# Performance work log

Measured on AMD Instinct MI355X. Metric: run time of the kernel, lower is better.

The kernel has to match this reference:

```python
import jax, jax.numpy as jnp
import numpy as np

N_NODES = 50000
N_EDGES = 800000
D = 128


def setup_inputs() -> dict:
    key = jax.random.key(0)
    ks = jax.random.split(key, 6)
    x = jax.random.normal(ks[0], (N_NODES, D), dtype=jnp.float32)
    edge_index = jax.random.randint(ks[1], (2, N_EDGES), 0, N_NODES, dtype=jnp.int32)
    scale = 1.0 / np.sqrt(D)
    W0 = jax.random.normal(ks[2], (D, D), dtype=jnp.float32) * scale
    W1 = jax.random.normal(ks[3], (D, D), dtype=jnp.float32) * scale
    W2 = jax.random.normal(ks[4], (D, D), dtype=jnp.float32) * scale
    b0 = jnp.zeros((D,), jnp.float32)
    b1 = jnp.zeros((D,), jnp.float32)
    b2 = jnp.zeros((D,), jnp.float32)
    return {"x": x, "edge_index": edge_index, "W0": W0, "b0": b0,
            "W1": W1, "b1": b1, "W2": W2, "b2": b2}


def _gcn_norm(edge_index, n_nodes, dtype):
    # symmetric normalization D^-1/2 A D^-1/2, no self loops (add_self_loops=False)
    src, dst = edge_index[1], edge_index[0]  # adj_t: aggregate src -> dst
    deg = jax.ops.segment_sum(jnp.ones(src.shape, dtype), src, num_segments=n_nodes)
    dis = jnp.where(deg > 0, jax.lax.rsqrt(jnp.maximum(deg, 1.0)), 0.0)
    return src, dst, dis[src] * dis[dst]  # per-edge norm [E]


def _gcn_layer(x, W, b, src, dst, norm, n_nodes):
    h = x @ W                                   # [N, d_out]
    msg = h[src] * norm[:, None]                # gather + scale, [E, d_out]
    agg = jax.ops.segment_sum(msg, dst, num_segments=n_nodes)
    return agg + b


def reference(x, edge_index, W0, b0, W1, b1, W2, b2):
    n = x.shape[0]
    src, dst, norm = _gcn_norm(edge_index, n, x.dtype)
    h = jax.nn.relu(_gcn_layer(x, W0, b0, src, dst, norm, n))
    h = jax.nn.relu(_gcn_layer(h, W1, b1, src, dst, norm, n))
    return _gcn_layer(h, W2, b2, src, dst, norm, n)
```

## Files before the change

kernel.cpp:

```cpp
#include <hip/hip_runtime.h>
#include <hip/hip_bf16.h>

#define DFEAT 128
#define RSPLIT 16
#define SSPLIT 64

typedef __attribute__((ext_vector_type(8))) short short8;
typedef __attribute__((ext_vector_type(4))) float f32x4;

__device__ __forceinline__ ushort f2bf(float f) {
    uint u = __float_as_uint(f);
    u += 0x7FFF + ((u >> 16) & 1);
    return (ushort)(u >> 16);
}
__device__ __forceinline__ float bf_lo(uint v) { return __uint_as_float(v << 16); }
__device__ __forceinline__ float bf_hi(uint v) { return __uint_as_float(v & 0xFFFF0000u); }


__global__ __launch_bounds__(512) void histrank_kernel(const int* __restrict__ EI,
                                                       int* __restrict__ cnt_part,
                                                       int* __restrict__ deg_part,
                                                       int* __restrict__ erank,
                                                       int nedges, int nnodes,
                                                       int range, int slice) {
    extern __shared__ int lds[];
    int* hd = lds;
    int* hs = lds + range;
    const int r = blockIdx.x & (RSPLIT - 1);
    const int s = blockIdx.x / RSPLIT;
    const int base = r * range;
    for (int i = threadIdx.x; i < 2 * range; i += 512) lds[i] = 0;
    __syncthreads();

    const int e0 = s * slice;
    const int e1 = min(nedges, e0 + slice);
    for (int e = e0 + threadIdx.x; e < e1; e += 512) {
        int dst = EI[e];
        int src = EI[nedges + e];
        unsigned ud = (unsigned)(dst - base);
        unsigned us = (unsigned)(src - base);
        if (ud < (unsigned)range) erank[e] = atomicAdd(&hd[ud], 1);
        if (us < (unsigned)range) atomicAdd(&hs[us], 1);
    }
    __syncthreads();

    for (int i = threadIdx.x; i < range; i += 512) {
        int node = base + i;
        if (node < nnodes) {
            cnt_part[s * nnodes + node] = hd[i];
            deg_part[s * nnodes + node] = hs[i];
        }
    }
}

__global__ __launch_bounds__(1024) void scan1_kernel(int* __restrict__ cnt_part,
                                                     const int* __restrict__ deg_part,
                                                     int* __restrict__ offs,
                                                     int* __restrict__ bsums,
                                                     float* __restrict__ dis, int n) {
    __shared__ int sm[1024];
    int t = threadIdx.x;
    int g = blockIdx.x * 1024 + t;
    int c = 0;
    if (g < n) {
        int d = 0;
        #pragma unroll
        for (int s = 0; s < SSPLIT; ++s) {
            int v = cnt_part[s * n + g];
            cnt_part[s * n + g] = c;
            c += v;
            d += deg_part[s * n + g];
        }
        dis[g] = (d > 0) ? rsqrtf((float)d) : 0.0f;
    }
    sm[t] = c;
    __syncthreads();
    for (int off = 1; off < 1024; off <<= 1) {
        int add = (t >= off) ? sm[t - off] : 0;
        __syncthreads();
        sm[t] += add;
        __syncthreads();
    }
    if (g < n) offs[g + 1] = sm[t];
    if (t == 1023) bsums[blockIdx.x] = sm[1023];
}

__global__ __launch_bounds__(1024) void scan3_kernel(int* __restrict__ offs,
                                                     const int* __restrict__ bsums,
                                                     int n, int nb) {
    __shared__ int pre[64];
    int t = threadIdx.x;
    if (t < 64) {
        int v = (t < nb) ? bsums[t] : 0;
        for (int off = 1; off < 64; off <<= 1) {
            int u = __shfl_up(v, off);
            if (t >= off) v += u;
        }
        int ex = __shfl_up(v, 1);
        if (t == 0) ex = 0;
        pre[t] = ex;
    }
    __syncthreads();
    int add = pre[blockIdx.x];
    int g = blockIdx.x * 1024 + t;
    if (g < n) offs[g + 1] += add;
    if (blockIdx.x == 0 && t == 0) offs[0] = 0;
}

__global__ void fill_kernel(const int* __restrict__ EI, const int* __restrict__ offs,
                            const int* __restrict__ erank, const int* __restrict__ sprefix,
                            const float* __restrict__ dis, int2* __restrict__ edges,
                            int nedges, int nnodes, int slice) {
    int e = blockIdx.x * blockDim.x + threadIdx.x;
    if (e >= nedges) return;
    int dst = EI[e];
    int src = EI[nedges + e];
    int s = e / slice;
    int idx = offs[dst] + sprefix[s * nnodes + dst] + erank[e];
    float nm = dis[src] * dis[dst];
    edges[idx] = make_int2(src, __float_as_int(nm));
}

__global__ void prepw_kernel(const float* __restrict__ W0, const float* __restrict__ W1,
                             const float* __restrict__ W2, ushort* __restrict__ Wtb) {
    int i = blockIdx.x * 256 + threadIdx.x;
    int m = i >> 14, r = i & 16383;
    int n = r >> 7, k = r & 127;
    const float* W = (m == 0) ? W0 : (m == 1) ? W1 : W2;
    Wtb[i] = f2bf(W[k * DFEAT + n]);
}


template <int IN_F32>
__global__ __launch_bounds__(256) void gemm_mfma(const void* __restrict__ Xin,
                                                 const ushort* __restrict__ Wtb,
                                                 ushort* __restrict__ Hb, int nrows) {
    __shared__ ushort wlds[128 * 136];
    const int t = threadIdx.x;

    #pragma unroll
    for (int q = 0; q < 8; ++q) {
        int c = t + q * 256;
        int row = c >> 4, cr = c & 15;
        short8 v = *(const short8*)(Wtb + c * 8);
        *(short8*)(&wlds[row * 136 + cr * 8]) = v;
    }
    __syncthreads();

    const int lane = t & 63;
    const int r16 = lane & 15, g = lane >> 4;
    const int row = blockIdx.x * 64 + (t >> 6) * 16 + r16;
    const int srow = (row < nrows) ? row : (nrows - 1);

    short8 a[4];
    if (IN_F32) {
        const float* X = (const float*)Xin;
        #pragma unroll
        for (int kc = 0; kc < 4; ++kc) {
            const float* p = X + (size_t)srow * DFEAT + kc * 32 + g * 8;
            float4 f0 = *(const float4*)p;
            float4 f1 = *(const float4*)(p + 4);
            short8 s;
            s[0] = (short)f2bf(f0.x); s[1] = (short)f2bf(f0.y);
            s[2] = (short)f2bf(f0.z); s[3] = (short)f2bf(f0.w);
            s[4] = (short)f2bf(f1.x); s[5] = (short)f2bf(f1.y);
            s[6] = (short)f2bf(f1.z); s[7] = (short)f2bf(f1.w);
            a[kc] = s;
        }
    } else {
        const ushort* X = (const ushort*)Xin;
        #pragma unroll
        for (int kc = 0; kc < 4; ++kc)
            a[kc] = *(const short8*)(X + (size_t)srow * DFEAT + kc * 32 + g * 8);
    }

    f32x4 acc[8];
    #pragma unroll
    for (int nt = 0; nt < 8; ++nt) acc[nt] = (f32x4){0.f, 0.f, 0.f, 0.f};

    #pragma unroll
    for (int kc = 0; kc < 4; ++kc) {
        #pragma unroll
        for (int nt = 0; nt < 8; ++nt) {
            short8 b = *(const short8*)(&wlds[(nt * 16 + r16) * 136 + kc * 32 + g * 8]);
            acc[nt] = __builtin_amdgcn_mfma_f32_16x16x32_bf16(a[kc], b, acc[nt], 0, 0, 0);
        }
    }

    const int orow_base = blockIdx.x * 64 + (t >> 6) * 16 + g * 4;
    #pragma unroll
    for (int nt = 0; nt < 8; ++nt) {
        #pragma unroll
        for (int r = 0; r < 4; ++r) {
            int orow = orow_base + r;
            if (orow < nrows)
                Hb[(size_t)orow * DFEAT + nt * 16 + r16] = f2bf(acc[nt][r]);
        }
    }
}


template <int RELU, int OUT_F32>
__global__ __launch_bounds__(256) void agg_kernel(const ushort* __restrict__ H,
                                                  const int* __restrict__ offs,
                                                  const int2* __restrict__ edges,
                                                  const float* __restrict__ bias,
                                                  void* __restrict__ OUT, int nnodes) {
    int node = blockIdx.x * 4 + (threadIdx.x >> 6);
    if (node >= nnodes) return;
    int lane = threadIdx.x & 63;
    int half = lane >> 5;
    int l32 = lane & 31;
    int s = offs[node];
    int e = offs[node + 1];

    float a0 = 0.f, a1 = 0.f, a2 = 0.f, a3 = 0.f;
    float c0 = 0.f, c1 = 0.f, c2 = 0.f, c3 = 0.f;
    const ushort* __restrict__ Hp = H + l32 * 4;

    int i = s + half;
    for (; i + 2 < e; i += 4) {
        int2 er0 = edges[i];
        int2 er1 = edges[i + 2];
        uint2 v0 = *(const uint2*)(Hp + (size_t)er0.x * DFEAT);
        uint2 v1 = *(const uint2*)(Hp + (size_t)er1.x * DFEAT);
        float n0 = __int_as_float(er0.y);
        float n1 = __int_as_float(er1.y);
        a0 += n0 * bf_lo(v0.x); a1 += n0 * bf_hi(v0.x);
        a2 += n0 * bf_lo(v0.y); a3 += n0 * bf_hi(v0.y);
        c0 += n1 * bf_lo(v1.x); c1 += n1 * bf_hi(v1.x);
        c2 += n1 * bf_lo(v1.y); c3 += n1 * bf_hi(v1.y);
    }
    if (i < e) {
        int2 er0 = edges[i];
        uint2 v0 = *(const uint2*)(Hp + (size_t)er0.x * DFEAT);
        float n0 = __int_as_float(er0.y);
        a0 += n0 * bf_lo(v0.x); a1 += n0 * bf_hi(v0.x);
        a2 += n0 * bf_lo(v0.y); a3 += n0 * bf_hi(v0.y);
    }
    a0 += c0; a1 += c1; a2 += c2; a3 += c3;

    a0 += __shfl_xor(a0, 32);
    a1 += __shfl_xor(a1, 32);
    a2 += __shfl_xor(a2, 32);
    a3 += __shfl_xor(a3, 32);

    float4 b4 = *(const float4*)&bias[l32 * 4];
    a0 += b4.x; a1 += b4.y; a2 += b4.z; a3 += b4.w;
    if (RELU) {
        a0 = fmaxf(a0, 0.f); a1 = fmaxf(a1, 0.f);
        a2 = fmaxf(a2, 0.f); a3 = fmaxf(a3, 0.f);
    }
    if (half == 0) {
        if (OUT_F32) {
            *(float4*)((float*)OUT + (size_t)node * DFEAT + l32 * 4) =
                make_float4(a0, a1, a2, a3);
        } else {
            uint2 p;
            p.x = (uint)f2bf(a0) | ((uint)f2bf(a1) << 16);
            p.y = (uint)f2bf(a2) | ((uint)f2bf(a3) << 16);
            *(uint2*)((ushort*)OUT + (size_t)node * DFEAT + l32 * 4) = p;
        }
    }
}


extern "C" void kernel_launch(void* const* d_in, const int* in_sizes, int n_in,
                              void* d_out, int out_size, void* d_ws, size_t ws_size,
                              hipStream_t stream) {
    const float* x  = (const float*)d_in[0];
    const int*   EI = (const int*)d_in[1];
    const float* W0 = (const float*)d_in[2];
    const float* b0 = (const float*)d_in[3];
    const float* W1 = (const float*)d_in[4];
    const float* b1 = (const float*)d_in[5];
    const float* W2 = (const float*)d_in[6];
    const float* b2 = (const float*)d_in[7];
    float* out = (float*)d_out;

    const int N = in_sizes[0] / DFEAT;
    const int E = in_sizes[1] / 2;
    const int range = (N + RSPLIT - 1) / RSPLIT;
    const int slice = (E + SSPLIT - 1) / SSPLIT;

    char* w = (char*)d_ws;
    auto alloc = [&](size_t bytes) {
        void* p = (void*)w;
        w += (bytes + 255) & ~(size_t)255;
        return p;
    };
    int*    offs  = (int*)alloc((size_t)(N + 1) * 4);
    int*    bsums = (int*)alloc(64 * 4);
    float*  dis   = (float*)alloc((size_t)N * 4);
    int*    erank = (int*)alloc((size_t)E * 4);
    int2*   edges = (int2*)alloc((size_t)E * 8);
    ushort* Wtb   = (ushort*)alloc((size_t)3 * DFEAT * DFEAT * 2);
    ushort* hbuf  = (ushort*)alloc((size_t)N * DFEAT * 2);
    ushort* abuf  = (ushort*)alloc((size_t)N * DFEAT * 2);

    int* cnt_part = (int*)hbuf;
    int* deg_part = (int*)abuf;

    const int nb = (N + 1023) / 1024;

    prepw_kernel<<<(3 * DFEAT * DFEAT) / 256, 256, 0, stream>>>(W0, W1, W2, Wtb);
    histrank_kernel<<<RSPLIT * SSPLIT, 512, 2 * range * 4, stream>>>(
        EI, cnt_part, deg_part, erank, E, N, range, slice);
    scan1_kernel<<<nb, 1024, 0, stream>>>(cnt_part, deg_part, offs, bsums, dis, N);
    scan3_kernel<<<nb, 1024, 0, stream>>>(offs, bsums, N, nb);
    fill_kernel<<<(E + 255) / 256, 256, 0, stream>>>(EI, offs, erank, cnt_part, dis,
                                                     edges, E, N, slice);

    const int gemmGrid = (N + 63) / 64;
    const int aggGrid  = (N + 3) / 4;

    gemm_mfma<1><<<gemmGrid, 256, 0, stream>>>(x, Wtb, hbuf, N);
    agg_kernel<1, 0><<<aggGrid, 256, 0, stream>>>(hbuf, offs, edges, b0, abuf, N);
    gemm_mfma<0><<<gemmGrid, 256, 0, stream>>>(abuf, Wtb + DFEAT * DFEAT, hbuf, N);
    agg_kernel<1, 0><<<aggGrid, 256, 0, stream>>>(hbuf, offs, edges, b1, abuf, N);
    gemm_mfma<0><<<gemmGrid, 256, 0, stream>>>(abuf, Wtb + 2 * DFEAT * DFEAT, hbuf, N);
    agg_kernel<0, 1><<<aggGrid, 256, 0, stream>>>(hbuf, offs, edges, b2, out, N);
}
```

Baseline: 221.4 us.

## Factor GCN norm into per-node scaling and widen aggregation gathers

```diff
diff --git a/kernel.cpp b/kernel.cpp
--- a/kernel.cpp
+++ b/kernel.cpp
@@ -2,7 +2,7 @@
 #include <hip/hip_bf16.h>
 
 #define DFEAT 128
-#define RSPLIT 16
+#define RSPLIT 8
 #define SSPLIT 64
 
 typedef __attribute__((ext_vector_type(8))) short short8;
@@ -109,16 +109,14 @@
 
 __global__ void fill_kernel(const int* __restrict__ EI, const int* __restrict__ offs,
                             const int* __restrict__ erank, const int* __restrict__ sprefix,
-                            const float* __restrict__ dis, int2* __restrict__ edges,
-                            int nedges, int nnodes, int slice) {
+                            int* __restrict__ esrc, int nedges, int nnodes, int slice) {
     int e = blockIdx.x * blockDim.x + threadIdx.x;
     if (e >= nedges) return;
     int dst = EI[e];
     int src = EI[nedges + e];
     int s = e / slice;
     int idx = offs[dst] + sprefix[s * nnodes + dst] + erank[e];
-    float nm = dis[src] * dis[dst];
-    edges[idx] = make_int2(src, __float_as_int(nm));
+    esrc[idx] = src;
 }
 
 __global__ void prepw_kernel(const float* __restrict__ W0, const float* __restrict__ W1,
@@ -134,6 +132,7 @@
 template <int IN_F32>
 __global__ __launch_bounds__(256) void gemm_mfma(const void* __restrict__ Xin,
                                                  const ushort* __restrict__ Wtb,
+                                                 const float* __restrict__ dis,
                                                  ushort* __restrict__ Hb, int nrows) {
     __shared__ ushort wlds[128 * 136];
     const int t = threadIdx.x;
@@ -145,56 +144,68 @@
         short8 v = *(const short8*)(Wtb + c * 8);
         *(short8*)(&wlds[row * 136 + cr * 8]) = v;
     }
-    __syncthreads();
 
     const int lane = t & 63;
     const int r16 = lane & 15, g = lane >> 4;
-    const int row = blockIdx.x * 64 + (t >> 6) * 16 + r16;
-    const int srow = (row < nrows) ? row : (nrows - 1);
-
-    short8 a[4];
-    if (IN_F32) {
-        const float* X = (const float*)Xin;
+    const int wv = t >> 6;
+    const int rbase = blockIdx.x * 128 + wv * 16;
+
+    short8 a[2][4];
+    #pragma unroll
+    for (int rt = 0; rt < 2; ++rt) {
+        int row = rbase + rt * 64 + r16;
+        int srow = (row < nrows) ? row : (nrows - 1);
+        if (IN_F32) {
+            const float* X = (const float*)Xin;
+            #pragma unroll
+            for (int kc = 0; kc < 4; ++kc) {
+                const float* p = X + (size_t)srow * DFEAT + kc * 32 + g * 8;
+                float4 f0 = *(const float4*)p;
+                float4 f1 = *(const float4*)(p + 4);
+                short8 sv;
+                sv[0] = (short)f2bf(f0.x); sv[1] = (short)f2bf(f0.y);
+                sv[2] = (short)f2bf(f0.z); sv[3] = (short)f2bf(f0.w);
+                sv[4] = (short)f2bf(f1.x); sv[5] = (short)f2bf(f1.y);
+                sv[6] = (short)f2bf(f1.z); sv[7] = (short)f2bf(f1.w);
+                a[rt][kc] = sv;
+            }
+        } else {
+            const ushort* X = (const ushort*)Xin;
+            #pragma unroll
+            for (int kc = 0; kc < 4; ++kc)
+                a[rt][kc] = *(const short8*)(X + (size_t)srow * DFEAT + kc * 32 + g * 8);
+        }
+    }
+    __syncthreads();
+
+    f32x4 acc[2][8];
+    #pragma unroll
+    for (int rt = 0; rt < 2; ++rt)
         #pragma unroll
-        for (int kc = 0; kc < 4; ++kc) {
-            const float* p = X + (size_t)srow * DFEAT + kc * 32 + g * 8;
-            float4 f0 = *(const float4*)p;
-            float4 f1 = *(const float4*)(p + 4);
-            short8 s;
-            s[0] = (short)f2bf(f0.x); s[1] = (short)f2bf(f0.y);
-            s[2] = (short)f2bf(f0.z); s[3] = (short)f2bf(f0.w);
-            s[4] = (short)f2bf(f1.x); s[5] = (short)f2bf(f1.y);
-            s[6] = (short)f2bf(f1.z); s[7] = (short)f2bf(f1.w);
-            a[kc] = s;
-        }
-    } else {
-        const ushort* X = (const ushort*)Xin;
-        #pragma unroll
-        for (int kc = 0; kc < 4; ++kc)
-            a[kc] = *(const short8*)(X + (size_t)srow * DFEAT + kc * 32 + g * 8);
-    }
-
-    f32x4 acc[8];
-    #pragma unroll
-    for (int nt = 0; nt < 8; ++nt) acc[nt] = (f32x4){0.f, 0.f, 0.f, 0.f};
+        for (int nt = 0; nt < 8; ++nt) acc[rt][nt] = (f32x4){0.f, 0.f, 0.f, 0.f};
 
     #pragma unroll
     for (int kc = 0; kc < 4; ++kc) {
         #pragma unroll
         for (int nt = 0; nt < 8; ++nt) {
             short8 b = *(const short8*)(&wlds[(nt * 16 + r16) * 136 + kc * 32 + g * 8]);
-            acc[nt] = __builtin_amdgcn_mfma_f32_16x16x32_bf16(a[kc], b, acc[nt], 0, 0, 0);
-        }
-    }
-
-    const int orow_base = blockIdx.x * 64 + (t >> 6) * 16 + g * 4;
-    #pragma unroll
-    for (int nt = 0; nt < 8; ++nt) {
+            acc[0][nt] = __builtin_amdgcn_mfma_f32_16x16x32_bf16(a[0][kc], b, acc[0][nt], 0, 0, 0);
+            acc[1][nt] = __builtin_amdgcn_mfma_f32_16x16x32_bf16(a[1][kc], b, acc[1][nt], 0, 0, 0);
+        }
+    }
+
+    #pragma unroll
+    for (int rt = 0; rt < 2; ++rt) {
+        const int orow_base = rbase + rt * 64 + g * 4;
         #pragma unroll
         for (int r = 0; r < 4; ++r) {
             int orow = orow_base + r;
-            if (orow < nrows)
-                Hb[(size_t)orow * DFEAT + nt * 16 + r16] = f2bf(acc[nt][r]);
+            if (orow < nrows) {
+                float d = dis[orow];
+                #pragma unroll
+                for (int nt = 0; nt < 8; ++nt)
+                    Hb[(size_t)orow * DFEAT + nt * 16 + r16] = f2bf(acc[rt][nt][r] * d);
+            }
         }
     }
 }
@@ -203,63 +214,84 @@
 template <int RELU, int OUT_F32>
 __global__ __launch_bounds__(256) void agg_kernel(const ushort* __restrict__ H,
                                                   const int* __restrict__ offs,
-                                                  const int2* __restrict__ edges,
+                                                  const int* __restrict__ esrc,
+                                                  const float* __restrict__ dis,
                                                   const float* __restrict__ bias,
                                                   void* __restrict__ OUT, int nnodes) {
     int node = blockIdx.x * 4 + (threadIdx.x >> 6);
     if (node >= nnodes) return;
     int lane = threadIdx.x & 63;
-    int half = lane >> 5;
-    int l32 = lane & 31;
+    int q = lane >> 4;
+    int l16 = lane & 15;
     int s = offs[node];
     int e = offs[node + 1];
 
     float a0 = 0.f, a1 = 0.f, a2 = 0.f, a3 = 0.f;
+    float a4 = 0.f, a5 = 0.f, a6 = 0.f, a7 = 0.f;
     float c0 = 0.f, c1 = 0.f, c2 = 0.f, c3 = 0.f;
-    const ushort* __restrict__ Hp = H + l32 * 4;
-
-    int i = s + half;
-    for (; i + 2 < e; i += 4) {
-        int2 er0 = edges[i];
-        int2 er1 = edges[i + 2];
-        uint2 v0 = *(const uint2*)(Hp + (size_t)er0.x * DFEAT);
-        uint2 v1 = *(const uint2*)(Hp + (size_t)er1.x * DFEAT);
-        float n0 = __int_as_float(er0.y);
-        float n1 = __int_as_float(er1.y);
-        a0 += n0 * bf_lo(v0.x); a1 += n0 * bf_hi(v0.x);
-        a2 += n0 * bf_lo(v0.y); a3 += n0 * bf_hi(v0.y);
-        c0 += n1 * bf_lo(v1.x); c1 += n1 * bf_hi(v1.x);
-        c2 += n1 * bf_lo(v1.y); c3 += n1 * bf_hi(v1.y);
+    float c4 = 0.f, c5 = 0.f, c6 = 0.f, c7 = 0.f;
+    const ushort* __restrict__ Hp = H + l16 * 8;
+
+    int i = s + q;
+    for (; i + 4 < e; i += 8) {
+        int s0 = esrc[i];
+        int s1 = esrc[i + 4];
+        uint4 v0 = *(const uint4*)(Hp + (size_t)s0 * DFEAT);
+        uint4 v1 = *(const uint4*)(Hp + (size_t)s1 * DFEAT);
+        a0 += bf_lo(v0.x); a1 += bf_hi(v0.x);
+        a2 += bf_lo(v0.y); a3 += bf_hi(v0.y);
+        a4 += bf_lo(v0.z); a5 += bf_hi(v0.z);
+        a6 += bf_lo(v0.w); a7 += bf_hi(v0.w);
+        c0 += bf_lo(v1.x); c1 += bf_hi(v1.x);
+        c2 += bf_lo(v1.y); c3 += bf_hi(v1.y);
+        c4 += bf_lo(v1.z); c5 += bf_hi(v1.z);
+        c6 += bf_lo(v1.w); c7 += bf_hi(v1.w);
     }
     if (i < e) {
-        int2 er0 = edges[i];
-        uint2 v0 = *(const uint2*)(Hp + (size_t)er0.x * DFEAT);
-        float n0 = __int_as_float(er0.y);
-        a0 += n0 * bf_lo(v0.x); a1 += n0 * bf_hi(v0.x);
-        a2 += n0 * bf_lo(v0.y); a3 += n0 * bf_hi(v0.y);
+        int s0 = esrc[i];
+        uint4 v0 = *(const uint4*)(Hp + (size_t)s0 * DFEAT);
+        a0 += bf_lo(v0.x); a1 += bf_hi(v0.x);
+        a2 += bf_lo(v0.y); a3 += bf_hi(v0.y);
+        a4 += bf_lo(v0.z); a5 += bf_hi(v0.z);
+        a6 += bf_lo(v0.w); a7 += bf_hi(v0.w);
     }
     a0 += c0; a1 += c1; a2 += c2; a3 += c3;
-
-    a0 += __shfl_xor(a0, 32);
-    a1 += __shfl_xor(a1, 32);
-    a2 += __shfl_xor(a2, 32);
-    a3 += __shfl_xor(a3, 32);
-
-    float4 b4 = *(const float4*)&bias[l32 * 4];
-    a0 += b4.x; a1 += b4.y; a2 += b4.z; a3 += b4.w;
+    a4 += c4; a5 += c5; a6 += c6; a7 += c7;
+
+    a0 += __shfl_xor(a0, 16); a1 += __shfl_xor(a1, 16);
+    a2 += __shfl_xor(a2, 16); a3 += __shfl_xor(a3, 16);
+    a4 += __shfl_xor(a4, 16); a5 += __shfl_xor(a5, 16);
+    a6 += __shfl_xor(a6, 16); a7 += __shfl_xor(a7, 16);
+    a0 += __shfl_xor(a0, 32); a1 += __shfl_xor(a1, 32);
+    a2 += __shfl_xor(a2, 32); a3 += __shfl_xor(a3, 32);
+    a4 += __shfl_xor(a4, 32); a5 += __shfl_xor(a5, 32);
+    a6 += __shfl_xor(a6, 32); a7 += __shfl_xor(a7, 32);
+
+    float dn = dis[node];
+    float4 b0 = *(const float4*)&bias[l16 * 8];
+    float4 b1 = *(const float4*)&bias[l16 * 8 + 4];
+    float r0 = dn * a0 + b0.x, r1 = dn * a1 + b0.y;
+    float r2 = dn * a2 + b0.z, r3 = dn * a3 + b0.w;
+    float r4 = dn * a4 + b1.x, r5 = dn * a5 + b1.y;
+    float r6 = dn * a6 + b1.z, r7 = dn * a7 + b1.w;
     if (RELU) {
-        a0 = fmaxf(a0, 0.f); a1 = fmaxf(a1, 0.f);
-        a2 = fmaxf(a2, 0.f); a3 = fmaxf(a3, 0.f);
-    }
-    if (half == 0) {
+        r0 = fmaxf(r0, 0.f); r1 = fmaxf(r1, 0.f);
+        r2 = fmaxf(r2, 0.f); r3 = fmaxf(r3, 0.f);
+        r4 = fmaxf(r4, 0.f); r5 = fmaxf(r5, 0.f);
+        r6 = fmaxf(r6, 0.f); r7 = fmaxf(r7, 0.f);
+    }
+    if (q == 0) {
         if (OUT_F32) {
-            *(float4*)((float*)OUT + (size_t)node * DFEAT + l32 * 4) =
-                make_float4(a0, a1, a2, a3);
+            float* o = (float*)OUT + (size_t)node * DFEAT + l16 * 8;
+            *(float4*)o = make_float4(r0, r1, r2, r3);
+            *(float4*)(o + 4) = make_float4(r4, r5, r6, r7);
         } else {
-            uint2 p;
-            p.x = (uint)f2bf(a0) | ((uint)f2bf(a1) << 16);
-            p.y = (uint)f2bf(a2) | ((uint)f2bf(a3) << 16);
-            *(uint2*)((ushort*)OUT + (size_t)node * DFEAT + l32 * 4) = p;
+            uint4 p;
+            p.x = (uint)f2bf(r0) | ((uint)f2bf(r1) << 16);
+            p.y = (uint)f2bf(r2) | ((uint)f2bf(r3) << 16);
+            p.z = (uint)f2bf(r4) | ((uint)f2bf(r5) << 16);
+            p.w = (uint)f2bf(r6) | ((uint)f2bf(r7) << 16);
+            *(uint4*)((ushort*)OUT + (size_t)node * DFEAT + l16 * 8) = p;
         }
     }
 }
@@ -293,7 +325,7 @@
     int*    bsums = (int*)alloc(64 * 4);
     float*  dis   = (float*)alloc((size_t)N * 4);
     int*    erank = (int*)alloc((size_t)E * 4);
-    int2*   edges = (int2*)alloc((size_t)E * 8);
+    int*    esrc  = (int*)alloc((size_t)E * 4);
     ushort* Wtb   = (ushort*)alloc((size_t)3 * DFEAT * DFEAT * 2);
     ushort* hbuf  = (ushort*)alloc((size_t)N * DFEAT * 2);
     ushort* abuf  = (ushort*)alloc((size_t)N * DFEAT * 2);
@@ -308,16 +340,16 @@
         EI, cnt_part, deg_part, erank, E, N, range, slice);
     scan1_kernel<<<nb, 1024, 0, stream>>>(cnt_part, deg_part, offs, bsums, dis, N);
     scan3_kernel<<<nb, 1024, 0, stream>>>(offs, bsums, N, nb);
-    fill_kernel<<<(E + 255) / 256, 256, 0, stream>>>(EI, offs, erank, cnt_part, dis,
-                                                     edges, E, N, slice);
-
-    const int gemmGrid = (N + 63) / 64;
+    fill_kernel<<<(E + 255) / 256, 256, 0, stream>>>(EI, offs, erank, cnt_part,
+                                                     esrc, E, N, slice);
+
+    const int gemmGrid = (N + 127) / 128;
     const int aggGrid  = (N + 3) / 4;
 
-    gemm_mfma<1><<<gemmGrid, 256, 0, stream>>>(x, Wtb, hbuf, N);
-    agg_kernel<1, 0><<<aggGrid, 256, 0, stream>>>(hbuf, offs, edges, b0, abuf, N);
-    gemm_mfma<0><<<gemmGrid, 256, 0, stream>>>(abuf, Wtb + DFEAT * DFEAT, hbuf, N);
-    agg_kernel<1, 0><<<aggGrid, 256, 0, stream>>>(hbuf, offs, edges, b1, abuf, N);
-    gemm_mfma<0><<<gemmGrid, 256, 0, stream>>>(abuf, Wtb + 2 * DFEAT * DFEAT, hbuf, N);
-    agg_kernel<0, 1><<<aggGrid, 256, 0, stream>>>(hbuf, offs, edges, b2, out, N);
-}
+    gemm_mfma<1><<<gemmGrid, 256, 0, stream>>>(x, Wtb, dis, hbuf, N);
+    agg_kernel<1, 0><<<aggGrid, 256, 0, stream>>>(hbuf, offs, esrc, dis, b0, abuf, N);
+    gemm_mfma<0><<<gemmGrid, 256, 0, stream>>>(abuf, Wtb + DFEAT * DFEAT, dis, hbuf, N);
+    agg_kernel<1, 0><<<aggGrid, 256, 0, stream>>>(hbuf, offs, esrc, dis, b1, abuf, N);
+    gemm_mfma<0><<<gemmGrid, 256, 0, stream>>>(abuf, Wtb + 2 * DFEAT * DFEAT, dis, hbuf, N);
+    agg_kernel<0, 1><<<aggGrid, 256, 0, stream>>>(hbuf, offs, esrc, dis, b2, out, N);
+}
```

Result: faster. 205.9 us (-7.0%).
